# Kernel tuning notes

Measured on AMD Instinct MI355X. Metric: run time of the kernel, lower is better.

## Reference

```python
import jax, jax.numpy as jnp
import numpy as np

N = 100000   # nodes
E = 1600000  # edges
F_IN, HID, OUT, K, L = 16, 128, 4, 3, 3


def setup_inputs() -> dict:
    key = jax.random.key(0)
    ks = jax.random.split(key, 16)
    x = jax.random.normal(ks[0], (N, F_IN), dtype=jnp.float32)
    edge_index = jax.random.randint(ks[1], (2, E), 0, N, dtype=jnp.int64)
    edge_attr = jax.random.uniform(ks[2], (E, 1), dtype=jnp.float32)
    s = 0.05
    # TAGConv l: K+1 stacked weight mats [K+1, in, out] + bias [out]
    W0 = jax.random.normal(ks[3], (K + 1, F_IN, HID), dtype=jnp.float32) * s
    b0 = jnp.zeros((HID,), dtype=jnp.float32)
    W1 = jax.random.normal(ks[4], (K + 1, HID, HID), dtype=jnp.float32) * s
    b1 = jnp.zeros((HID,), dtype=jnp.float32)
    W2 = jax.random.normal(ks[5], (K + 1, HID, HID), dtype=jnp.float32) * s
    b2 = jnp.zeros((HID,), dtype=jnp.float32)
    Wfc = jax.random.normal(ks[6], (HID, OUT), dtype=jnp.float32) * s
    bfc = jnp.zeros((OUT,), dtype=jnp.float32)
    return dict(x=x, edge_index=edge_index, edge_attr=edge_attr,
                W0=W0, b0=b0, W1=W1, b1=b1, W2=W2, b2=b2, Wfc=Wfc, bfc=bfc)


def _gcn_norm(row, col, edge_weight, num_nodes):
    # PyG gcn_norm with add_self_loops=False: deg over target (col)
    deg = jax.ops.segment_sum(edge_weight, col, num_segments=num_nodes)
    dis = jnp.where(deg > 0, 1.0 / jnp.sqrt(deg), 0.0)  # masked_fill inf -> 0
    return dis[row] * edge_weight * dis[col]  # [E]


def _tagconv(x, row, col, norm, W, b, num_nodes):
    # out = sum_k lin_k(A_norm^k x) + b
    out = x @ W[0]
    h = x
    for k in range(1, W.shape[0]):
        h = jax.ops.segment_sum(norm[:, None] * h[row], col, num_segments=num_nodes)
        out = out + h @ W[k]
    return out + b


def reference(x, edge_index, edge_attr, W0, b0, W1, b1, W2, b2, Wfc, bfc):
    row, col = edge_index[0], edge_index[1]
    ew = edge_attr.squeeze()
    norm = _gcn_norm(row, col, ew, N)
    h = x
    # layers 0..L-2: conv + (dropout p=0 identity) + relu
    for W, b in ((W0, b0), (W1, b1)):
        h = jax.nn.relu(_tagconv(h, row, col, norm, W, b, N))
    h = _tagconv(h, row, col, norm, W2, b2, N)
    return h @ Wfc + bfc
```

## Files before the change

kernel.cpp:

```cpp
#include <hip/hip_runtime.h>
#include <cstddef>
#include <cstdint>

#define NN 100000
#define NE 1600000

typedef unsigned short u16;
using short8 = __attribute__((ext_vector_type(8))) short;
using f32x4  = __attribute__((ext_vector_type(4))) float;

__device__ inline u16 f2bf(float f) {
    unsigned u = __float_as_uint(f);
    unsigned r = u + 0x7fffu + ((u >> 16) & 1u);
    return (u16)(r >> 16);
}
__device__ inline float bflo(unsigned u) { return __uint_as_float(u << 16); }
__device__ inline float bfhi(unsigned u) { return __uint_as_float(u & 0xffff0000u); }


__global__ void count_k(const int* __restrict__ col, int* __restrict__ cnt,
                        int* __restrict__ rank) {
    int e = blockIdx.x * 256 + threadIdx.x;
    int c = col[e];
    rank[e] = atomicAdd(&cnt[c], 1);
}

__global__ void scan1_k(const int* __restrict__ cnt, int* __restrict__ exc,
                        int* __restrict__ blksum) {
    __shared__ int sm[256];
    int i = blockIdx.x * 256 + threadIdx.x;
    int v = (i < NN) ? cnt[i] : 0;
    sm[threadIdx.x] = v;
    __syncthreads();
    for (int off = 1; off < 256; off <<= 1) {
        int t = (threadIdx.x >= off) ? sm[threadIdx.x - off] : 0;
        __syncthreads();
        sm[threadIdx.x] += t;
        __syncthreads();
    }
    if (i < NN) exc[i] = sm[threadIdx.x] - v;
    if (threadIdx.x == 255) blksum[blockIdx.x] = sm[255];
}

__global__ void scan2_k(int* __restrict__ blksum, int nb) {
    __shared__ int sm[512];
    int t = threadIdx.x;
    int v = (t < nb) ? blksum[t] : 0;
    sm[t] = v;
    __syncthreads();
    for (int off = 1; off < 512; off <<= 1) {
        int x = (t >= off) ? sm[t - off] : 0;
        __syncthreads();
        sm[t] += x;
        __syncthreads();
    }
    if (t < nb) blksum[t] = sm[t] - v;
}

__global__ void scan3_k(int* __restrict__ rowptr, const int* __restrict__ blksum) {
    int i = blockIdx.x * 256 + threadIdx.x;
    if (i < NN) rowptr[i] += blksum[blockIdx.x];
    if (i == 0) rowptr[NN] = NE;
}

__global__ void scatter_k(const int* __restrict__ row, const int* __restrict__ col,
                          const float* __restrict__ ew, const int* __restrict__ rowptr,
                          const int* __restrict__ rank, int2* __restrict__ epair) {
    int e = blockIdx.x * 256 + threadIdx.x;
    int c = col[e];
    int p = rowptr[c] + rank[e];
    int2 pr;
    pr.x = row[e];
    pr.y = __float_as_int(ew[e]);
    epair[p] = pr;
}

__global__ void dis_k(const int* __restrict__ rowptr, const int2* __restrict__ epair,
                      float* __restrict__ dis) {
    int v = blockIdx.x * 256 + threadIdx.x;
    if (v >= NN) return;
    int s = rowptr[v], e = rowptr[v + 1];
    float d = 0.f;
    for (int i = s; i < e; ++i) d += __int_as_float(epair[i].y);
    dis[v] = (d > 0.f) ? (1.0f / sqrtf(d)) : 0.f;
}

__global__ void norm_k(const int* __restrict__ rowptr, const float* __restrict__ dis,
                       int2* __restrict__ epair) {
    int v = blockIdx.x * 256 + threadIdx.x;
    if (v >= NN) return;
    float dv = dis[v];
    int s = rowptr[v], e = rowptr[v + 1];
    int* ey = (int*)epair;
    for (int i = s; i < e; ++i) {
        int2 p = epair[i];
        float w = dis[p.x] * __int_as_float(p.y) * dv;
        ey[2 * i + 1] = __float_as_int(w);
    }
}

template <int K>
__global__ void wt_k(const float* __restrict__ W, u16* __restrict__ Wt) {
    int id = blockIdx.x * 256 + threadIdx.x;
    int j = id / K, k = id % K;
    Wt[(size_t)j * K + k] = f2bf(W[(size_t)k * 128 + j]);
}


__global__ void prop16_k(const float* __restrict__ hin, float* __restrict__ hout,
                         const int* __restrict__ rowptr, const int2* __restrict__ epair) {
    int t = blockIdx.x * 256 + threadIdx.x;
    int v = t >> 2, q = t & 3;
    if (v >= NN) return;
    int s = rowptr[v], e = rowptr[v + 1];
    const float* __restrict__ hq = hin + q * 4;
    float4 a0 = make_float4(0.f, 0.f, 0.f, 0.f);
    float4 a1 = make_float4(0.f, 0.f, 0.f, 0.f);
    int i = s;
    for (; i + 3 < e; i += 4) {
        int2 p0 = epair[i];
        int2 p1 = epair[i + 1];
        int2 p2 = epair[i + 2];
        int2 p3 = epair[i + 3];
        float4 h0 = *reinterpret_cast<const float4*>(hq + (size_t)p0.x * 16);
        float4 h1 = *reinterpret_cast<const float4*>(hq + (size_t)p1.x * 16);
        float4 h2 = *reinterpret_cast<const float4*>(hq + (size_t)p2.x * 16);
        float4 h3 = *reinterpret_cast<const float4*>(hq + (size_t)p3.x * 16);
        float w0 = __int_as_float(p0.y), w1 = __int_as_float(p1.y);
        float w2 = __int_as_float(p2.y), w3 = __int_as_float(p3.y);
        a0.x += w0 * h0.x; a0.y += w0 * h0.y; a0.z += w0 * h0.z; a0.w += w0 * h0.w;
        a1.x += w1 * h1.x; a1.y += w1 * h1.y; a1.z += w1 * h1.z; a1.w += w1 * h1.w;
        a0.x += w2 * h2.x; a0.y += w2 * h2.y; a0.z += w2 * h2.z; a0.w += w2 * h2.w;
        a1.x += w3 * h3.x; a1.y += w3 * h3.y; a1.z += w3 * h3.z; a1.w += w3 * h3.w;
    }
    for (; i < e; ++i) {
        int2 p = epair[i];
        float w = __int_as_float(p.y);
        float4 h = *reinterpret_cast<const float4*>(hq + (size_t)p.x * 16);
        a0.x += w * h.x; a0.y += w * h.y; a0.z += w * h.z; a0.w += w * h.w;
    }
    float4 acc = make_float4(a0.x + a1.x, a0.y + a1.y, a0.z + a1.z, a0.w + a1.w);
    *reinterpret_cast<float4*>(hout + (size_t)v * 16 + q * 4) = acc;
}

__global__ void pack_k(const float* __restrict__ x, const float* __restrict__ p1,
                       const float* __restrict__ p2, const float* __restrict__ p3,
                       u16* __restrict__ Xcat) {
    int id = blockIdx.x * 256 + threadIdx.x;
    if (id >= NN * 4) return;
    int v = id >> 2, s = id & 3;
    const float* src = (s == 0 ? x : s == 1 ? p1 : s == 2 ? p2 : p3) + (size_t)v * 16;
    unsigned* dst = (unsigned*)(Xcat + (size_t)v * 64 + s * 16);
#pragma unroll
    for (int f = 0; f < 8; ++f) {
        dst[f] = (unsigned)f2bf(src[2 * f]) | ((unsigned)f2bf(src[2 * f + 1]) << 16);
    }
}

__global__ __launch_bounds__(256) void propbf_k(
    const u16* __restrict__ hin, u16* __restrict__ hout,
    const int* __restrict__ rowptr, const int2* __restrict__ epair) {
    int wid = (blockIdx.x * 256 + threadIdx.x) >> 6;
    int lane = threadIdx.x & 63;
    int g = lane >> 4;
    int l = lane & 15;
    int v = __builtin_amdgcn_readfirstlane(wid);
    int s = rowptr[v], e = rowptr[v + 1];
    const u16* __restrict__ hb = hin + l * 8;
    float a[8];
#pragma unroll
    for (int k = 0; k < 8; ++k) a[k] = 0.f;

    int i = s;
    for (; i + 7 < e; i += 8) {
        int2 pa = epair[i + g];
        int2 pb = epair[i + 4 + g];
        uint4 ha = *(const uint4*)(hb + (size_t)pa.x * 512);
        uint4 hc = *(const uint4*)(hb + (size_t)pb.x * 512);
        float wa = __int_as_float(pa.y), wb = __int_as_float(pb.y);
        a[0] += wa * bflo(ha.x); a[1] += wa * bfhi(ha.x);
        a[2] += wa * bflo(ha.y); a[3] += wa * bfhi(ha.y);
        a[4] += wa * bflo(ha.z); a[5] += wa * bfhi(ha.z);
        a[6] += wa * bflo(ha.w); a[7] += wa * bfhi(ha.w);
        a[0] += wb * bflo(hc.x); a[1] += wb * bfhi(hc.x);
        a[2] += wb * bflo(hc.y); a[3] += wb * bfhi(hc.y);
        a[4] += wb * bflo(hc.z); a[5] += wb * bfhi(hc.z);
        a[6] += wb * bflo(hc.w); a[7] += wb * bfhi(hc.w);
    }
    for (; i < e; i += 4) {
        int idx = i + g;
        int2 p = (idx < e) ? epair[idx] : make_int2(0, 0);
        uint4 h = *(const uint4*)(hb + (size_t)p.x * 512);
        float w = __int_as_float(p.y);
        a[0] += w * bflo(h.x); a[1] += w * bfhi(h.x);
        a[2] += w * bflo(h.y); a[3] += w * bfhi(h.y);
        a[4] += w * bflo(h.z); a[5] += w * bfhi(h.z);
        a[6] += w * bflo(h.w); a[7] += w * bfhi(h.w);
    }
#pragma unroll
    for (int k = 0; k < 8; ++k) {
        a[k] += __shfl_xor(a[k], 16);
        a[k] += __shfl_xor(a[k], 32);
    }
    if (g == 0) {
        uint4 o;
        o.x = (unsigned)f2bf(a[0]) | ((unsigned)f2bf(a[1]) << 16);
        o.y = (unsigned)f2bf(a[2]) | ((unsigned)f2bf(a[3]) << 16);
        o.z = (unsigned)f2bf(a[4]) | ((unsigned)f2bf(a[5]) << 16);
        o.w = (unsigned)f2bf(a[6]) | ((unsigned)f2bf(a[7]) << 16);
        *(uint4*)(hout + (size_t)v * 512 + l * 8) = o;
    }
}

template <int KSTEPS, int RELU>
__global__ __launch_bounds__(512, 2) void mgemm2_k(
    const u16* __restrict__ A, const u16* __restrict__ Bt,
    const float* __restrict__ bias, u16* __restrict__ outb,
    int* __restrict__ ctr, int ntiles) {
    const int K = KSTEPS * 32;
    const int BBYTES = 128 * K * 2;
    __shared__ u16 smB[128 * KSTEPS * 32];
    __shared__ int smt;
    int tid = threadIdx.x;

    for (int d = tid * 16; d < BBYTES; d += 512 * 16) {
        int rowb = d / (K * 2);
        int src = d ^ ((rowb & 7) << 4);
        *(short8*)((char*)smB + d) = *(const short8*)((const char*)Bt + src);
    }

    int lane = tid & 63;
    int wv = tid >> 6;
    int r = lane & 15, h = lane >> 4;
    float bj[8];
#pragma unroll
    for (int j = 0; j < 8; ++j) bj[j] = bias[j * 16 + r];
    const char* bbase = (const char*)smB;

    for (;;) {
        __syncthreads();
        if (tid == 0) smt = atomicAdd(ctr, 1);
        __syncthreads();
        int t = smt;
        if (t >= ntiles) break;
        int v0 = t * 256 + wv * 32;
        if (v0 >= NN) continue;

        const u16* a0p = A + (size_t)(v0 + r) * K + h * 8;
        const u16* a1p = a0p + (size_t)16 * K;
        f32x4 acc0[8], acc1[8];
#pragma unroll
        for (int j = 0; j < 8; ++j) {
            acc0[j] = {0.f, 0.f, 0.f, 0.f};
            acc1[j] = {0.f, 0.f, 0.f, 0.f};
        }
#pragma unroll
        for (int kk = 0; kk < KSTEPS; ++kk) {
            short8 a0 = *(const short8*)(a0p + kk * 32);
            short8 a1 = *(const short8*)(a1p + kk * 32);
#pragma unroll
            for (int j = 0; j < 8; ++j) {
                int bb = ((j * 16 + r) * K * 2 + kk * 64 + h * 16) ^ ((r & 7) << 4);
                short8 b = *(const short8*)(bbase + bb);
                acc0[j] = __builtin_amdgcn_mfma_f32_16x16x32_bf16(a0, b, acc0[j], 0, 0, 0);
                acc1[j] = __builtin_amdgcn_mfma_f32_16x16x32_bf16(a1, b, acc1[j], 0, 0, 0);
            }
        }
#pragma unroll
        for (int i = 0; i < 4; ++i) {
            int row0 = v0 + h * 4 + i;
#pragma unroll
            for (int j = 0; j < 8; ++j) {
                float c0 = acc0[j][i] + bj[j];
                float c1 = acc1[j][i] + bj[j];
                if (RELU) { c0 = fmaxf(c0, 0.f); c1 = fmaxf(c1, 0.f); }
                outb[(size_t)row0 * 512 + j * 16 + r] = f2bf(c0);
                outb[(size_t)(row0 + 16) * 512 + j * 16 + r] = f2bf(c1);
            }
        }
    }
}

__global__ void fcb_k(const u16* __restrict__ H, const float* __restrict__ Wfc,
                      const float* __restrict__ bfc, float* __restrict__ out) {
    int t = blockIdx.x * 256 + threadIdx.x;
    int v = t >> 6, p = t & 63;
    unsigned u = *(const unsigned*)(H + (size_t)v * 512 + p * 2);
    float h0 = bflo(u), h1 = bfhi(u);
    float4 w0 = reinterpret_cast<const float4*>(Wfc)[2 * p];
    float4 w1 = reinterpret_cast<const float4*>(Wfc)[2 * p + 1];
    float s0 = h0 * w0.x + h1 * w1.x;
    float s1 = h0 * w0.y + h1 * w1.y;
    float s2 = h0 * w0.z + h1 * w1.z;
    float s3 = h0 * w0.w + h1 * w1.w;
#pragma unroll
    for (int off = 32; off; off >>= 1) {
        s0 += __shfl_xor(s0, off);
        s1 += __shfl_xor(s1, off);
        s2 += __shfl_xor(s2, off);
        s3 += __shfl_xor(s3, off);
    }
    if (p == 0) {
        float4 o = make_float4(s0 + bfc[0], s1 + bfc[1], s2 + bfc[2], s3 + bfc[3]);
        reinterpret_cast<float4*>(out)[v] = o;
    }
}


extern "C" void kernel_launch(void* const* d_in, const int* in_sizes, int n_in,
                              void* d_out, int out_size, void* d_ws, size_t ws_size,
                              hipStream_t stream) {
    const float* x    = (const float*)d_in[0];
    const int*   ei   = (const int*)d_in[1];
    const float* ea   = (const float*)d_in[2];
    const float* W0   = (const float*)d_in[3];
    const float* b0   = (const float*)d_in[4];
    const float* W1   = (const float*)d_in[5];
    const float* b1   = (const float*)d_in[6];
    const float* W2   = (const float*)d_in[7];
    const float* b2   = (const float*)d_in[8];
    const float* Wfc  = (const float*)d_in[9];
    const float* bfc  = (const float*)d_in[10];
    float* out = (float*)d_out;

    const int* row = ei;
    const int* col = ei + NE;

    char* w = (char*)d_ws;
    size_t off = 0;
    auto alloc = [&](size_t bytes) {
        size_t o = off;
        off += (bytes + 255) & ~(size_t)255;
        return (void*)(w + o);
    };
    int*   cnt    = (int*)  alloc((size_t)NN * 4);
    int*   ctr    = (int*)  alloc(3 * 4);
    size_t zero_bytes = off;
    int*   rowptr = (int*)  alloc((size_t)(NN + 1) * 4);
    int*   blksum = (int*)  alloc(512 * 4);
    float* dis    = (float*)alloc((size_t)NN * 4);
    int2*  epair  = (int2*) alloc((size_t)NE * 8);
    u16*   Wt0    = (u16*)  alloc((size_t)128 * 64 * 2);
    u16*   Wt1    = (u16*)  alloc((size_t)128 * 512 * 2);
    u16*   Wt2    = (u16*)  alloc((size_t)128 * 512 * 2);
    char*  ureg   = (char*) alloc((size_t)NN * 128 * 4);
    float* P1   = (float*)(ureg);
    float* P2   = (float*)(ureg + (size_t)NN * 16 * 4);
    float* P3   = (float*)(ureg + (size_t)NN * 32 * 4);
    u16*   Xcat = (u16*)  (ureg + (size_t)NN * 48 * 4);
    u16*   Hcat = (u16*)  alloc((size_t)NN * 512 * 2);
    int*   rank = (int*)Hcat;
    (void)ws_size;

    const int nScanB = (NN + 255) / 256;
    const int nEdgeB = NE / 256;
    const int nPropB = NN * 64 / 256;
    const int nTiles = (NN + 255) / 256;

    hipMemsetAsync(cnt, 0, zero_bytes, stream);
    count_k<<<nEdgeB, 256, 0, stream>>>(col, cnt, rank);
    scan1_k<<<nScanB, 256, 0, stream>>>(cnt, rowptr, blksum);
    scan2_k<<<1, 512, 0, stream>>>(blksum, nScanB);
    scan3_k<<<nScanB, 256, 0, stream>>>(rowptr, blksum);
    scatter_k<<<nEdgeB, 256, 0, stream>>>(row, col, ea, rowptr, rank, epair);
    dis_k<<<nScanB, 256, 0, stream>>>(rowptr, epair, dis);
    norm_k<<<nScanB, 256, 0, stream>>>(rowptr, dis, epair);

    wt_k<64> <<<32,  256, 0, stream>>>(W0, Wt0);
    wt_k<512><<<256, 256, 0, stream>>>(W1, Wt1);
    wt_k<512><<<256, 256, 0, stream>>>(W2, Wt2);

    const int n16B = (NN * 4 + 255) / 256;
    prop16_k<<<n16B, 256, 0, stream>>>(x,  P1, rowptr, epair);
    prop16_k<<<n16B, 256, 0, stream>>>(P1, P2, rowptr, epair);
    prop16_k<<<n16B, 256, 0, stream>>>(P2, P3, rowptr, epair);
    pack_k<<<n16B, 256, 0, stream>>>(x, P1, P2, P3, Xcat);
    mgemm2_k<2, 1><<<256, 512, 0, stream>>>(Xcat, Wt0, b0, Hcat, ctr + 0, nTiles);

    propbf_k<<<nPropB, 256, 0, stream>>>(Hcat,       Hcat + 128, rowptr, epair);
    propbf_k<<<nPropB, 256, 0, stream>>>(Hcat + 128, Hcat + 256, rowptr, epair);
    propbf_k<<<nPropB, 256, 0, stream>>>(Hcat + 256, Hcat + 384, rowptr, epair);
    mgemm2_k<16, 1><<<256, 512, 0, stream>>>(Hcat, Wt1, b1, Hcat, ctr + 1, nTiles);

    propbf_k<<<nPropB, 256, 0, stream>>>(Hcat,       Hcat + 128, rowptr, epair);
    propbf_k<<<nPropB, 256, 0, stream>>>(Hcat + 128, Hcat + 256, rowptr, epair);
    propbf_k<<<nPropB, 256, 0, stream>>>(Hcat + 256, Hcat + 384, rowptr, epair);
    mgemm2_k<16, 0><<<256, 512, 0, stream>>>(Hcat, Wt2, b2, Hcat, ctr + 2, nTiles);

    fcb_k<<<nPropB, 256, 0, stream>>>(Hcat, Wfc, bfc, out);
}
```

Before: 681.0 us.

## Build CSR via two-level bucketed radix partition instead of global atomics

Replaces the CSR construction, which used a global atomic count, a multi-kernel scan and a random scatter, with a two-pass bucket partition. Edges are first histogrammed into 64-node buckets in shared memory and partitioned into contiguous bucket regions. Each bucket is then sorted locally in shared memory, and the degree normalisation is computed in the same pass. This is meant to cut global atomic contention and scattered writes, at the cost of an extra edge buffer and more kernel launches. It also relies on every bucket holding at most 3072 edges (12 per thread), which holds only for roughly uniform degree distributions.

```diff
diff --git a/kernel.cpp b/kernel.cpp
--- a/kernel.cpp
+++ b/kernel.cpp
@@ -4,6 +4,11 @@
 
 #define NN 100000
 #define NE 1600000
+
+#define CB 1563
+#define CBP 1568
+#define EPB 4096
+#define A1B 391
 
 typedef unsigned short u16;
 using short8 = __attribute__((ext_vector_type(8))) short;
@@ -18,71 +23,139 @@
 __device__ inline float bfhi(unsigned u) { return __uint_as_float(u & 0xffff0000u); }
 
 
-__global__ void count_k(const int* __restrict__ col, int* __restrict__ cnt,
-                        int* __restrict__ rank) {
-    int e = blockIdx.x * 256 + threadIdx.x;
-    int c = col[e];
-    rank[e] = atomicAdd(&cnt[c], 1);
-}
-
-__global__ void scan1_k(const int* __restrict__ cnt, int* __restrict__ exc,
-                        int* __restrict__ blksum) {
-    __shared__ int sm[256];
-    int i = blockIdx.x * 256 + threadIdx.x;
-    int v = (i < NN) ? cnt[i] : 0;
-    sm[threadIdx.x] = v;
+__global__ __launch_bounds__(256) void hist_k(const int* __restrict__ col,
+                                              unsigned* __restrict__ M) {
+    __shared__ unsigned h[CBP];
+    for (int i = threadIdx.x; i < CBP; i += 256) h[i] = 0;
+    __syncthreads();
+    int base = blockIdx.x * EPB;
+    for (int i = threadIdx.x; i < EPB; i += 256) {
+        int e = base + i;
+        if (e < NE) atomicAdd(&h[col[e] >> 6], 1u);
+    }
+    __syncthreads();
+    unsigned* mrow = M + (size_t)blockIdx.x * CBP;
+    for (int i = threadIdx.x; i < CBP; i += 256) mrow[i] = h[i];
+}
+
+__global__ __launch_bounds__(256) void totals_k(const unsigned* __restrict__ M,
+                                                unsigned* __restrict__ tot) {
+    int b = blockIdx.x * 256 + threadIdx.x;
+    if (b >= CBP) return;
+    unsigned s = 0;
+    for (int r = 0; r < A1B; ++r) s += M[(size_t)r * CBP + b];
+    tot[b] = s;
+}
+
+__global__ __launch_bounds__(256) void scanb_k(const unsigned* __restrict__ tot,
+                                               unsigned* __restrict__ cb) {
+    __shared__ unsigned part[256];
+    int t = threadIdx.x;
+    unsigned loc[7];
+    unsigned s = 0;
+#pragma unroll
+    for (int k = 0; k < 7; ++k) {
+        int i = t * 7 + k;
+        unsigned v = (i < CBP) ? tot[i] : 0;
+        loc[k] = s; s += v;
+    }
+    part[t] = s;
     __syncthreads();
     for (int off = 1; off < 256; off <<= 1) {
-        int t = (threadIdx.x >= off) ? sm[threadIdx.x - off] : 0;
-        __syncthreads();
-        sm[threadIdx.x] += t;
-        __syncthreads();
-    }
-    if (i < NN) exc[i] = sm[threadIdx.x] - v;
-    if (threadIdx.x == 255) blksum[blockIdx.x] = sm[255];
-}
-
-__global__ void scan2_k(int* __restrict__ blksum, int nb) {
-    __shared__ int sm[512];
+        unsigned x = (t >= off) ? part[t - off] : 0;
+        __syncthreads();
+        part[t] += x;
+        __syncthreads();
+    }
+    unsigned base = (t > 0) ? part[t - 1] : 0;
+#pragma unroll
+    for (int k = 0; k < 7; ++k) {
+        int i = t * 7 + k;
+        if (i <= CBP) cb[i] = base + loc[k];
+    }
+}
+
+__global__ __launch_bounds__(256) void base_k(const unsigned* __restrict__ cb,
+                                              unsigned* __restrict__ M) {
+    int b = blockIdx.x * 256 + threadIdx.x;
+    if (b >= CBP) return;
+    unsigned run = cb[b];
+    for (int r = 0; r < A1B; ++r) {
+        unsigned v = M[(size_t)r * CBP + b];
+        M[(size_t)r * CBP + b] = run;
+        run += v;
+    }
+}
+
+__global__ __launch_bounds__(256) void part_k(const int* __restrict__ row,
+                                              const int* __restrict__ col,
+                                              const float* __restrict__ ew,
+                                              const unsigned* __restrict__ M,
+                                              int2* __restrict__ Abuf) {
+    __shared__ unsigned cur[CBP];
+    const unsigned* mrow = M + (size_t)blockIdx.x * CBP;
+    for (int i = threadIdx.x; i < CBP; i += 256) cur[i] = mrow[i];
+    __syncthreads();
+    int base = blockIdx.x * EPB;
+    for (int i = threadIdx.x; i < EPB; i += 256) {
+        int e = base + i;
+        if (e < NE) {
+            int c = col[e];
+            unsigned pos = atomicAdd(&cur[c >> 6], 1u);
+            Abuf[pos] = make_int2(row[e] | ((c & 63) << 17), __float_as_int(ew[e]));
+        }
+    }
+}
+
+__global__ __launch_bounds__(256) void build_k(const int2* __restrict__ Abuf,
+                                               const unsigned* __restrict__ cb,
+                                               int* __restrict__ rowptr,
+                                               int2* __restrict__ epair,
+                                               float* __restrict__ dis) {
+    int b = blockIdx.x;
     int t = threadIdx.x;
-    int v = (t < nb) ? blksum[t] : 0;
-    sm[t] = v;
-    __syncthreads();
-    for (int off = 1; off < 512; off <<= 1) {
-        int x = (t >= off) ? sm[t - off] : 0;
-        __syncthreads();
-        sm[t] += x;
-        __syncthreads();
-    }
-    if (t < nb) blksum[t] = sm[t] - v;
-}
-
-__global__ void scan3_k(int* __restrict__ rowptr, const int* __restrict__ blksum) {
-    int i = blockIdx.x * 256 + threadIdx.x;
-    if (i < NN) rowptr[i] += blksum[blockIdx.x];
-    if (i == 0) rowptr[NN] = NE;
-}
-
-__global__ void scatter_k(const int* __restrict__ row, const int* __restrict__ col,
-                          const float* __restrict__ ew, const int* __restrict__ rowptr,
-                          const int* __restrict__ rank, int2* __restrict__ epair) {
-    int e = blockIdx.x * 256 + threadIdx.x;
-    int c = col[e];
-    int p = rowptr[c] + rank[e];
-    int2 pr;
-    pr.x = row[e];
-    pr.y = __float_as_int(ew[e]);
-    epair[p] = pr;
-}
-
-__global__ void dis_k(const int* __restrict__ rowptr, const int2* __restrict__ epair,
-                      float* __restrict__ dis) {
-    int v = blockIdx.x * 256 + threadIdx.x;
-    if (v >= NN) return;
-    int s = rowptr[v], e = rowptr[v + 1];
-    float d = 0.f;
-    for (int i = s; i < e; ++i) d += __int_as_float(epair[i].y);
-    dis[v] = (d > 0.f) ? (1.0f / sqrtf(d)) : 0.f;
+    __shared__ int cnt[64];
+    __shared__ int offs[64];
+    __shared__ int ex[64];
+    __shared__ float dsum[64];
+    if (t < 64) { cnt[t] = 0; dsum[t] = 0.f; }
+    __syncthreads();
+    unsigned s = cb[b], e = cb[b + 1];
+    int n = (int)(e - s);
+    int2 mye[12]; int myb[12]; int myn = 0;
+    for (int i = t; i < n; i += 256) {
+        int2 p = Abuf[s + i];
+        int cl = (p.x >> 17) & 63;
+        if (myn < 12) { mye[myn] = p; myb[myn] = cl; ++myn; }
+        atomicAdd(&cnt[cl], 1);
+        atomicAdd(&dsum[cl], __int_as_float(p.y));
+    }
+    __syncthreads();
+    if (t < 64) offs[t] = cnt[t];
+    __syncthreads();
+    for (int off = 1; off < 64; off <<= 1) {
+        int x = 0;
+        if (t < 64 && t >= off) x = offs[t - off];
+        __syncthreads();
+        if (t < 64) offs[t] += x;
+        __syncthreads();
+    }
+    if (t < 64) { ex[t] = offs[t] - cnt[t]; cnt[t] = 0; }
+    __syncthreads();
+    for (int k = 0; k < myn; ++k) {
+        int cl = myb[k];
+        int r = atomicAdd(&cnt[cl], 1);
+        epair[s + ex[cl] + r] = make_int2(mye[k].x & 0x1FFFF, mye[k].y);
+    }
+    if (t < 64) {
+        int v = b * 64 + t;
+        if (v < NN) {
+            rowptr[v] = (int)s + ex[t];
+            float d = dsum[t];
+            dis[v] = (d > 0.f) ? (1.0f / sqrtf(d)) : 0.f;
+        }
+    }
+    if (b == CB - 1 && t == 0) rowptr[NN] = NE;
 }
 
 __global__ void norm_k(const int* __restrict__ rowptr, const float* __restrict__ dis,
@@ -91,11 +164,10 @@
     if (v >= NN) return;
     float dv = dis[v];
     int s = rowptr[v], e = rowptr[v + 1];
-    int* ey = (int*)epair;
     for (int i = s; i < e; ++i) {
         int2 p = epair[i];
         float w = dis[p.x] * __int_as_float(p.y) * dv;
-        ey[2 * i + 1] = __float_as_int(w);
+        epair[i] = make_int2(p.x, __float_as_int(w));
     }
 }
 
@@ -333,38 +405,40 @@
         off += (bytes + 255) & ~(size_t)255;
         return (void*)(w + o);
     };
-    int*   cnt    = (int*)  alloc((size_t)NN * 4);
-    int*   ctr    = (int*)  alloc(3 * 4);
+    int*      ctr    = (int*)     alloc(3 * 4);
     size_t zero_bytes = off;
-    int*   rowptr = (int*)  alloc((size_t)(NN + 1) * 4);
-    int*   blksum = (int*)  alloc(512 * 4);
-    float* dis    = (float*)alloc((size_t)NN * 4);
-    int2*  epair  = (int2*) alloc((size_t)NE * 8);
-    u16*   Wt0    = (u16*)  alloc((size_t)128 * 64 * 2);
-    u16*   Wt1    = (u16*)  alloc((size_t)128 * 512 * 2);
-    u16*   Wt2    = (u16*)  alloc((size_t)128 * 512 * 2);
-    char*  ureg   = (char*) alloc((size_t)NN * 128 * 4);
+    int*      rowptr = (int*)     alloc((size_t)(NN + 1) * 4);
+    float*    dis    = (float*)   alloc((size_t)NN * 4);
+    unsigned* M      = (unsigned*)alloc((size_t)A1B * CBP * 4);
+    unsigned* tot    = (unsigned*)alloc((size_t)CBP * 4);
+    unsigned* cb     = (unsigned*)alloc((size_t)(CBP + 1) * 4);
+    int2*     Abuf   = (int2*)    alloc((size_t)NE * 8);
+    int2*     epair  = (int2*)    alloc((size_t)NE * 8);
+    u16*      Wt0    = (u16*)     alloc((size_t)128 * 64 * 2);
+    u16*      Wt1    = (u16*)     alloc((size_t)128 * 512 * 2);
+    u16*      Wt2    = (u16*)     alloc((size_t)128 * 512 * 2);
+    char*     ureg   = (char*)    alloc((size_t)NN * 128 * 4);
     float* P1   = (float*)(ureg);
     float* P2   = (float*)(ureg + (size_t)NN * 16 * 4);
     float* P3   = (float*)(ureg + (size_t)NN * 32 * 4);
     u16*   Xcat = (u16*)  (ureg + (size_t)NN * 48 * 4);
-    u16*   Hcat = (u16*)  alloc((size_t)NN * 512 * 2);
-    int*   rank = (int*)Hcat;
+    u16*      Hcat   = (u16*)     alloc((size_t)NN * 512 * 2);
     (void)ws_size;
 
     const int nScanB = (NN + 255) / 256;
-    const int nEdgeB = NE / 256;
     const int nPropB = NN * 64 / 256;
     const int nTiles = (NN + 255) / 256;
-
-    hipMemsetAsync(cnt, 0, zero_bytes, stream);
-    count_k<<<nEdgeB, 256, 0, stream>>>(col, cnt, rank);
-    scan1_k<<<nScanB, 256, 0, stream>>>(cnt, rowptr, blksum);
-    scan2_k<<<1, 512, 0, stream>>>(blksum, nScanB);
-    scan3_k<<<nScanB, 256, 0, stream>>>(rowptr, blksum);
-    scatter_k<<<nEdgeB, 256, 0, stream>>>(row, col, ea, rowptr, rank, epair);
-    dis_k<<<nScanB, 256, 0, stream>>>(rowptr, epair, dis);
-    norm_k<<<nScanB, 256, 0, stream>>>(rowptr, dis, epair);
+    const int nBkt   = (CBP + 255) / 256;
+
+    hipMemsetAsync(ctr, 0, zero_bytes, stream);
+
+    hist_k  <<<A1B,  256, 0, stream>>>(col, M);
+    totals_k<<<nBkt, 256, 0, stream>>>(M, tot);
+    scanb_k <<<1,    256, 0, stream>>>(tot, cb);
+    base_k  <<<nBkt, 256, 0, stream>>>(cb, M);
+    part_k  <<<A1B,  256, 0, stream>>>(row, col, ea, M, Abuf);
+    build_k <<<CB,   256, 0, stream>>>(Abuf, cb, rowptr, epair, dis);
+    norm_k  <<<nScanB, 256, 0, stream>>>(rowptr, dis, epair);
 
     wt_k<64> <<<32,  256, 0, stream>>>(W0, Wt0);
     wt_k<512><<<256, 256, 0, stream>>>(W1, Wt1);
```

Result: faster. 653.9 us (-4.0%).
